# Kernel optimization log

Hardware: AMD Instinct MI355X
Metric: run time of the kernel (lower is better)

Reference implementation:

```python
import jax, jax.numpy as jnp
import numpy as np

NH, NKV, D = 8, 2, 256
EPS = 1e-6
SCALING = 1.0 / 256.0  # query_rescale_scalar / query_pre_attn_scalar


def _rms(x):
    # Gemma3nRMSNorm with with_scale=False: x / sqrt(mean(x^2) + eps)
    return x * jax.lax.rsqrt(jnp.mean(x * x, axis=-1, keepdims=True) + EPS)


def _rotate_half(x):
    h = x.shape[-1] // 2
    return jnp.concatenate([-x[..., h:], x[..., :h]], axis=-1)


def setup_inputs() -> dict:
    key = jax.random.key(0)
    ks = jax.random.split(key, 5)
    S, H = 4096, 2048
    hidden_states = jax.random.normal(ks[0], (S, H), dtype=jnp.float32)
    # realistic rope cos/sin
    pos = jnp.arange(S, dtype=jnp.float32)
    inv_freq = 1.0 / (10000.0 ** (jnp.arange(0, D, 2, dtype=jnp.float32) / D))
    ang = pos[:, None] * inv_freq[None, :]              # [S, D/2]
    emb = jnp.concatenate([ang, ang], axis=-1)          # [S, D]
    cos = jnp.cos(emb)
    sin = jnp.sin(emb)
    qkv_w = jax.random.normal(ks[1], ((NH + 2 * NKV) * D, H), dtype=jnp.float32) * 0.02
    o_w = jax.random.normal(ks[2], (H, NH * D), dtype=jnp.float32) * 0.02
    return {"hidden_states": hidden_states, "cos": cos, "sin": sin,
            "qkv_w": qkv_w, "o_w": o_w}


def reference(hidden_states, cos, sin, qkv_w, o_w):
    S = hidden_states.shape[0]
    qkv = hidden_states @ qkv_w.T                        # [S, (NH+2NKV)*D]
    q, k, v = jnp.split(qkv, [NH * D, (NH + NKV) * D], axis=-1)
    q = q.reshape(S, NH, D)                              # [S, NH, D]
    k = k.reshape(S, NKV, D)
    v = v.reshape(S, NKV, D)
    # per-head RMSNorm (no learned scale) on q, k, v
    q = _rms(q)
    k = _rms(k)
    v = _rms(v)
    # RoPE on q, k (v untouched)
    c = cos[:, None, :]
    s = sin[:, None, :]
    q = q * c + _rotate_half(q) * s
    k = k * c + _rotate_half(k) * s
    # GQA: expand kv heads to query heads
    rep = NH // NKV
    k = jnp.repeat(k, rep, axis=1)                       # [S, NH, D]
    v = jnp.repeat(v, rep, axis=1)
    scores = jnp.einsum('qhd,khd->hqk', q, k) * SCALING  # [NH, S, S]
    mask = jnp.tril(jnp.ones((S, S), dtype=bool))
    scores = jnp.where(mask[None], scores, jnp.finfo(scores.dtype).min)
    probs = jax.nn.softmax(scores, axis=-1)
    attn = jnp.einsum('hqk,khd->qhd', probs, v)          # [S, NH, D]
    out = attn.reshape(S, NH * D) @ o_w.T                # [S, H]
    return out
```

## Files before the change

kernel.cpp:

```cpp
#include <hip/hip_runtime.h>

#define NHEADS 8
#define NKVH   2
#define HD     256
#define SEQ    4096
#define HID    2048
#define QKVN   3072
#define SCAL   (1.0f/256.0f)
#define NITEMS 640

typedef __attribute__((ext_vector_type(8))) __bf16 bf16x8;
typedef __attribute__((ext_vector_type(4))) float  f32x4;

__device__ __forceinline__ unsigned short f2bf(float f) {
  unsigned int u = __builtin_bit_cast(unsigned int, f);
  u += 0x7fffu + ((u >> 16) & 1u);
  return (unsigned short)(u >> 16);
}
__device__ __forceinline__ float bf2f(unsigned short b) {
  return __builtin_bit_cast(float, (unsigned int)b << 16);
}

__device__ __forceinline__ void async_copy16(const void* g, void* l) {
  __builtin_amdgcn_global_load_lds(
      (__attribute__((address_space(1))) void*)(g),
      (__attribute__((address_space(3))) void*)(l), 16, 0, 0);
}

__device__ __forceinline__ int slot_prefix(int b) {
  if (b < 16) return 0;
  if (b < 32) return b - 16;
  if (b < 48) return 16 + 2 * (b - 32);
  return 48 + 3 * (b - 48);
}

__global__ __launch_bounds__(256) void cvt_bf16(const float* __restrict__ in,
                                                unsigned short* __restrict__ out,
                                                int n4) {
  int i = blockIdx.x * 256 + threadIdx.x;
  if (i >= n4) return;
  float4 v = reinterpret_cast<const float4*>(in)[i];
  ushort4 o;
  o.x = f2bf(v.x); o.y = f2bf(v.y); o.z = f2bf(v.z); o.w = f2bf(v.w);
  reinterpret_cast<ushort4*>(out)[i] = o;
}

template <bool OUT_BF16>
__global__ __launch_bounds__(256) void gemm_bt(const unsigned short* __restrict__ A,
                                               const unsigned short* __restrict__ B,
                                               void* __restrict__ C,
                                               int M, int N, int K) {
  __shared__ __align__(16) unsigned short Als[128 * 64];
  __shared__ __align__(16) unsigned short Bls[128 * 64];
  const int t    = threadIdx.x;
  const int lane = t & 63;
  const int wid  = t >> 6;
  const int wr = wid >> 1, wc = wid & 1;
  const int l15 = lane & 15, lg = lane >> 4;
  const int m0 = blockIdx.y * 128, n0 = blockIdx.x * 128;

  f32x4 acc[4][4] = {};

  for (int k0 = 0; k0 < K; k0 += 64) {
    __syncthreads();
#pragma unroll
    for (int i = 0; i < 4; ++i) {
      int c   = i * 256 + t;
      int kc  = c >> 9;
      int row = (c >> 2) & 127;
      int j8  = (c & 3) ^ (row & 3);
      int gcol = k0 + kc * 32 + j8 * 8;
      async_copy16(A + (size_t)(m0 + row) * K + gcol, Als + c * 8);
      async_copy16(B + (size_t)(n0 + row) * K + gcol, Bls + c * 8);
    }
    __syncthreads();
#pragma unroll
    for (int kc = 0; kc < 2; ++kc) {
      bf16x8 af[4], bfr[4];
#pragma unroll
      for (int m = 0; m < 4; ++m) {
        int row   = wr * 64 + m * 16 + l15;
        int chunk = kc * 512 + row * 4 + (lg ^ (row & 3));
        af[m] = *reinterpret_cast<const bf16x8*>(Als + chunk * 8);
      }
#pragma unroll
      for (int n = 0; n < 4; ++n) {
        int row   = wc * 64 + n * 16 + l15;
        int chunk = kc * 512 + row * 4 + (lg ^ (row & 3));
        bfr[n] = *reinterpret_cast<const bf16x8*>(Bls + chunk * 8);
      }
#pragma unroll
      for (int m = 0; m < 4; ++m)
#pragma unroll
        for (int n = 0; n < 4; ++n)
          acc[m][n] = __builtin_amdgcn_mfma_f32_16x16x32_bf16(af[m], bfr[n],
                                                              acc[m][n], 0, 0, 0);
    }
  }

#pragma unroll
  for (int m = 0; m < 4; ++m) {
#pragma unroll
    for (int n = 0; n < 4; ++n) {
      int col = n0 + wc * 64 + n * 16 + l15;
#pragma unroll
      for (int r = 0; r < 4; ++r) {
        int rowg = m0 + wr * 64 + m * 16 + lg * 4 + r;
        if constexpr (OUT_BF16)
          reinterpret_cast<unsigned short*>(C)[(size_t)rowg * N + col] =
              f2bf(acc[m][n][r]);
        else
          reinterpret_cast<float*>(C)[(size_t)rowg * N + col] = acc[m][n][r];
      }
    }
  }
}

__global__ __launch_bounds__(256) void postproc(const unsigned short* __restrict__ qkv,
                                                const float* __restrict__ cosb,
                                                const float* __restrict__ sinb,
                                                unsigned short* __restrict__ q,
                                                unsigned short* __restrict__ k,
                                                unsigned short* __restrict__ vt) {
  const int wid = threadIdx.x >> 6, lane = threadIdx.x & 63;
  const int task = blockIdx.x * 4 + wid;
  const int s = task / 12, comp = task % 12;

  ushort4 raw = reinterpret_cast<const ushort4*>(qkv + (size_t)task * 256)[lane];
  float x0 = bf2f(raw.x), x1 = bf2f(raw.y), x2 = bf2f(raw.z), x3 = bf2f(raw.w);

  float ss = x0 * x0 + x1 * x1 + x2 * x2 + x3 * x3;
#pragma unroll
  for (int m = 1; m < 64; m <<= 1) ss += __shfl_xor(ss, m);
  float inv = rsqrtf(ss * (1.0f / 256.0f) + 1e-6f);
  x0 *= inv; x1 *= inv; x2 *= inv; x3 *= inv;

  if (comp < 10) {
    float4 c  = reinterpret_cast<const float4*>(cosb + (size_t)s * 256)[lane];
    float4 sn = reinterpret_cast<const float4*>(sinb + (size_t)s * 256)[lane];
    float p0 = __shfl_xor(x0, 32), p1 = __shfl_xor(x1, 32);
    float p2 = __shfl_xor(x2, 32), p3 = __shfl_xor(x3, 32);
    float sg = (lane < 32) ? -1.0f : 1.0f;
    x0 = x0 * c.x + sg * p0 * sn.x;
    x1 = x1 * c.y + sg * p1 * sn.y;
    x2 = x2 * c.z + sg * p2 * sn.z;
    x3 = x3 * c.w + sg * p3 * sn.w;
  }

  if (comp < 8) {
    ushort4 o;
    o.x = f2bf(x0 * SCAL); o.y = f2bf(x1 * SCAL);
    o.z = f2bf(x2 * SCAL); o.w = f2bf(x3 * SCAL);
    reinterpret_cast<ushort4*>(q + ((size_t)s * NHEADS + comp) * 256)[lane] = o;
  } else if (comp < 10) {
    ushort4 o;
    o.x = f2bf(x0); o.y = f2bf(x1); o.z = f2bf(x2); o.w = f2bf(x3);
    reinterpret_cast<ushort4*>(k + ((size_t)(comp - 8) * SEQ + s) * 256)[lane] = o;
  } else {
    size_t base = (size_t)(comp - 10) * 1048576 + (size_t)(s >> 5) * 8192 +
                  (size_t)((s >> 3) & 3) * 2048 + (s & 7);
    int d0 = lane * 4;
    vt[base + (size_t)(d0 + 0) * 8] = f2bf(x0);
    vt[base + (size_t)(d0 + 1) * 8] = f2bf(x1);
    vt[base + (size_t)(d0 + 2) * 8] = f2bf(x2);
    vt[base + (size_t)(d0 + 3) * 8] = f2bf(x3);
  }
}

__global__ __launch_bounds__(256, 2) void flash(const unsigned short* __restrict__ q,
                                                const unsigned short* __restrict__ k,
                                                const unsigned short* __restrict__ vtg,
                                                unsigned short* __restrict__ attn,
                                                unsigned short* __restrict__ opart,
                                                float* __restrict__ ml0,
                                                float* __restrict__ mlp,
                                                int* __restrict__ ticket) {
  extern __shared__ __align__(16) unsigned short lds[];
  unsigned short* Kls = lds;
  unsigned short* Vls = lds + 16384;
  unsigned short* Pls = lds + 32768;
  __shared__ int s_item;

  const int tid  = threadIdx.x;
  const int lane = tid & 63, wid = tid >> 6;
  const int l15 = lane & 15, lg = lane >> 4;

  for (;;) {
    if (tid == 0) s_item = atomicAdd(ticket, 1);
    __syncthreads();
    const int it = s_item;
    __syncthreads();
    if (it >= NITEMS) break;

    int b, hp, j;
    if (it < 256)      { b = 63 - (it >> 4);          int r = it & 15;        hp = r >> 2; j = r & 3; }
    else if (it < 448) { int u = it - 256; b = 47 - u / 12; int r = u % 12;   hp = r / 3;  j = r % 3; }
    else if (it < 576) { int u = it - 448; b = 31 - (u >> 3); int r = u & 7;  hp = r >> 1; j = r & 1; }
    else               { int u = it - 576; b = 15 - (u >> 2); hp = u & 3;     j = 0; }

    const int h0 = hp * 2, kvh = hp >> 1;
    const int total_t = 2 * b + 2;
    const int t0 = j * 32;
    const int t1 = min(t0 + 32, total_t) - 1;
    const int qb = b * 64 + wid * 16;

    const unsigned short* kbase  = k   + (size_t)kvh * SEQ * 256;
    const unsigned short* vstage = vtg + (size_t)kvh * 1048576;

    bf16x8 qf[2][8];
#pragma unroll
    for (int g = 0; g < 2; ++g) {
      const unsigned short* qrow =
          q + ((size_t)(qb + l15) * NHEADS + h0 + g) * 256 + lg * 8;
#pragma unroll
      for (int kc = 0; kc < 8; ++kc)
        qf[g][kc] = *reinterpret_cast<const bf16x8*>(qrow + kc * 32);
    }

    f32x4 o[16][2];
#pragma unroll
    for (int i = 0; i < 16; ++i)
#pragma unroll
      for (int g = 0; g < 2; ++g) o[i][g] = f32x4{0.f, 0.f, 0.f, 0.f};
    float mr0 = -1e30f, lr0 = 0.f, mr1 = -1e30f, lr1 = 0.f;

    auto stage = [&](int bb, int t) {
      const int kvb = t * 32;
#pragma unroll
      for (int i = 0; i < 4; ++i) {
        int p = i * 256 + tid;
        int krow = p >> 5, pj = p & 31;
        int jj = (pj & ~7) | ((pj ^ krow) & 7);
        async_copy16(kbase + (size_t)(kvb + krow) * 256 + jj * 8,
                     Kls + bb * 8192 + p * 8);
      }
      const unsigned short* vsrc = vstage + (size_t)t * 8192;
#pragma unroll
      for (int i = 0; i < 4; ++i) {
        int p = i * 256 + tid;
        async_copy16(vsrc + p * 8, Vls + bb * 8192 + p * 8);
      }
    };

    int cur = 0;
    stage(0, t0);
    __syncthreads();

    for (int t = t0; t <= t1; ++t) {
      const int kvb = t * 32;
      if (t + 1 <= t1) stage(cur ^ 1, t + 1);

      if (kvb <= qb + 15) {
        const unsigned short* Kc = Kls + cur * 8192;
        const unsigned short* Vc = Vls + cur * 8192;

        f32x4 s[2][2] = {};
        __builtin_amdgcn_s_setprio(1);
#pragma unroll
        for (int n = 0; n < 2; ++n) {
          const int row = n * 16 + l15;
#pragma unroll
          for (int kc = 0; kc < 8; ++kc) {
            int jj = kc * 4 + lg;
            int pj = (jj & ~7) | ((jj ^ row) & 7);
            bf16x8 kf = *reinterpret_cast<const bf16x8*>(Kc + (row * 32 + pj) * 8);
            s[0][n] = __builtin_amdgcn_mfma_f32_16x16x32_bf16(kf, qf[0][kc], s[0][n], 0, 0, 0);
            s[1][n] = __builtin_amdgcn_mfma_f32_16x16x32_bf16(kf, qf[1][kc], s[1][n], 0, 0, 0);
          }
        }
        __builtin_amdgcn_s_setprio(0);

        if (kvb + 31 > qb) {
#pragma unroll
          for (int n = 0; n < 2; ++n)
#pragma unroll
            for (int r = 0; r < 4; ++r)
              if (kvb + n * 16 + lg * 4 + r > qb + l15) {
                s[0][n][r] = -1e30f;
                s[1][n][r] = -1e30f;
              }
        }

        float pm0 = fmaxf(fmaxf(fmaxf(s[0][0][0], s[0][0][1]), fmaxf(s[0][0][2], s[0][0][3])),
                          fmaxf(fmaxf(s[0][1][0], s[0][1][1]), fmaxf(s[0][1][2], s[0][1][3])));
        float pm1 = fmaxf(fmaxf(fmaxf(s[1][0][0], s[1][0][1]), fmaxf(s[1][0][2], s[1][0][3])),
                          fmaxf(fmaxf(s[1][1][0], s[1][1][1]), fmaxf(s[1][1][2], s[1][1][3])));
        pm0 = fmaxf(pm0, __shfl_xor(pm0, 16));
        pm0 = fmaxf(pm0, __shfl_xor(pm0, 32));
        pm1 = fmaxf(pm1, __shfl_xor(pm1, 16));
        pm1 = fmaxf(pm1, __shfl_xor(pm1, 32));

        if (__any(fmaxf(pm0 - mr0, pm1 - mr1) > 8.0f)) {
          float mn0 = fmaxf(mr0, pm0), mn1 = fmaxf(mr1, pm1);
          float sc0 = __expf(mr0 - mn0), sc1 = __expf(mr1 - mn1);
#pragma unroll
          for (int i = 0; i < 16; ++i)
#pragma unroll
            for (int r = 0; r < 4; ++r) {
              o[i][0][r] *= sc0;
              o[i][1][r] *= sc1;
            }
          lr0 *= sc0; lr1 *= sc1;
          mr0 = mn0;  mr1 = mn1;
        }

#pragma unroll
        for (int n = 0; n < 2; ++n)
#pragma unroll
          for (int r = 0; r < 4; ++r) {
            s[0][n][r] = __expf(s[0][n][r] - mr0);
            s[1][n][r] = __expf(s[1][n][r] - mr1);
          }

        float rs0 = ((s[0][0][0] + s[0][0][1]) + (s[0][0][2] + s[0][0][3])) +
                    ((s[0][1][0] + s[0][1][1]) + (s[0][1][2] + s[0][1][3]));
        float rs1 = ((s[1][0][0] + s[1][0][1]) + (s[1][0][2] + s[1][0][3])) +
                    ((s[1][1][0] + s[1][1][1]) + (s[1][1][2] + s[1][1][3]));
        rs0 += __shfl_xor(rs0, 16); rs0 += __shfl_xor(rs0, 32);
        rs1 += __shfl_xor(rs1, 16); rs1 += __shfl_xor(rs1, 32);
        lr0 += rs0; lr1 += rs1;

#pragma unroll
        for (int g = 0; g < 2; ++g) {
          unsigned short* Pr = Pls + ((wid * 2 + g) * 16 + l15) * 40;
#pragma unroll
          for (int n = 0; n < 2; ++n) {
            ushort4 w;
            w.x = f2bf(s[g][n][0]); w.y = f2bf(s[g][n][1]);
            w.z = f2bf(s[g][n][2]); w.w = f2bf(s[g][n][3]);
            *reinterpret_cast<ushort4*>(Pr + n * 16 + lg * 4) = w;
          }
        }
        asm volatile("s_waitcnt lgkmcnt(0)" ::: "memory");
        __builtin_amdgcn_sched_barrier(0);

        bf16x8 pb0 = *reinterpret_cast<const bf16x8*>(
            Pls + ((wid * 2 + 0) * 16 + l15) * 40 + lg * 8);
        bf16x8 pb1 = *reinterpret_cast<const bf16x8*>(
            Pls + ((wid * 2 + 1) * 16 + l15) * 40 + lg * 8);
        __builtin_amdgcn_s_setprio(1);
#pragma unroll
        for (int dt = 0; dt < 16; ++dt) {
          bf16x8 vf = *reinterpret_cast<const bf16x8*>(
              Vc + ((lg << 8) + dt * 16 + l15) * 8);
          o[dt][0] = __builtin_amdgcn_mfma_f32_16x16x32_bf16(vf, pb0, o[dt][0], 0, 0, 0);
          o[dt][1] = __builtin_amdgcn_mfma_f32_16x16x32_bf16(vf, pb1, o[dt][1], 0, 0, 0);
        }
        __builtin_amdgcn_s_setprio(0);
      }

      __syncthreads();
      cur ^= 1;
    }

    const int qrow = qb + l15;
#pragma unroll
    for (int g = 0; g < 2; ++g) {
      const int head = h0 + g;
      const float mg = g ? mr1 : mr0;
      const float lg_ = g ? lr1 : lr0;
      if (j == 0) {
#pragma unroll
        for (int dt = 0; dt < 16; ++dt) {
          ushort4 w;
          w.x = f2bf(o[dt][g][0]); w.y = f2bf(o[dt][g][1]);
          w.z = f2bf(o[dt][g][2]); w.w = f2bf(o[dt][g][3]);
          *reinterpret_cast<ushort4*>(
              attn + (size_t)qrow * HID + head * 256 + dt * 16 + lg * 4) = w;
        }
        if (lg == 0)
          reinterpret_cast<float2*>(ml0)[head * SEQ + qrow] = float2{mg, lg_};
      } else {
        const int p = slot_prefix(b) + (j - 1);
        const size_t prow = ((size_t)head * 96 + p) * 64 + (qrow & 63);
#pragma unroll
        for (int dt = 0; dt < 16; ++dt) {
          ushort4 w;
          w.x = f2bf(o[dt][g][0]); w.y = f2bf(o[dt][g][1]);
          w.z = f2bf(o[dt][g][2]); w.w = f2bf(o[dt][g][3]);
          *reinterpret_cast<ushort4*>(opart + prow * 256 + dt * 16 + lg * 4) = w;
        }
        if (lg == 0) reinterpret_cast<float2*>(mlp)[prow] = float2{mg, lg_};
      }
    }
    __syncthreads();
  }
}

__global__ __launch_bounds__(256) void merge(const unsigned short* __restrict__ opart,
                                             const float* __restrict__ ml0,
                                             const float* __restrict__ mlp,
                                             unsigned short* __restrict__ attn) {
  const int wid = threadIdx.x >> 6, lane = threadIdx.x & 63;
  const int rid = blockIdx.x * 4 + wid;
  const int h = rid >> 12, s = rid & 4095;
  const int b = s >> 6;
  const int n = (b >> 4) + 1;

  float2 m_l[4];
  m_l[0] = reinterpret_cast<const float2*>(ml0)[rid];
  const int pf = slot_prefix(b);
  size_t prow[4];
  for (int jj = 1; jj < n; ++jj) {
    prow[jj] = ((size_t)h * 96 + pf + jj - 1) * 64 + (s & 63);
    m_l[jj] = reinterpret_cast<const float2*>(mlp)[prow[jj]];
  }

  float M = m_l[0].x;
  for (int jj = 1; jj < n; ++jj) M = fmaxf(M, m_l[jj].x);
  float w[4], L = 0.f;
  for (int jj = 0; jj < n; ++jj) {
    w[jj] = __expf(m_l[jj].x - M);
    L += w[jj] * m_l[jj].y;
  }
  float invL = 1.0f / L;
  for (int jj = 0; jj < n; ++jj) w[jj] *= invL;

  unsigned short* arow = attn + (size_t)s * HID + h * 256;
  ushort4 a = reinterpret_cast<const ushort4*>(arow)[lane];
  float acc0 = w[0] * bf2f(a.x), acc1 = w[0] * bf2f(a.y);
  float acc2 = w[0] * bf2f(a.z), acc3 = w[0] * bf2f(a.w);
  for (int jj = 1; jj < n; ++jj) {
    ushort4 bq = reinterpret_cast<const ushort4*>(opart + prow[jj] * 256)[lane];
    acc0 += w[jj] * bf2f(bq.x); acc1 += w[jj] * bf2f(bq.y);
    acc2 += w[jj] * bf2f(bq.z); acc3 += w[jj] * bf2f(bq.w);
  }
  ushort4 o;
  o.x = f2bf(acc0); o.y = f2bf(acc1); o.z = f2bf(acc2); o.w = f2bf(acc3);
  reinterpret_cast<ushort4*>(arow)[lane] = o;
}

extern "C" void kernel_launch(void* const* d_in, const int* in_sizes, int n_in,
                              void* d_out, int out_size, void* d_ws, size_t ws_size,
                              hipStream_t stream) {
  const float* hs   = (const float*)d_in[0];
  const float* cosb = (const float*)d_in[1];
  const float* sinb = (const float*)d_in[2];
  const float* qkvw = (const float*)d_in[3];
  const float* ow   = (const float*)d_in[4];

  char* ws = (char*)d_ws;
  unsigned short* hs_bf   = (unsigned short*)(ws + 0);
  unsigned short* wqkv_bf = (unsigned short*)(ws + 16777216);
  unsigned short* wo_bf   = (unsigned short*)(ws + 29360128);
  unsigned short* qkv_bf  = (unsigned short*)(ws + 37748736);
  unsigned short* attn_bf = qkv_bf;
  unsigned short* q_bf    = (unsigned short*)(ws + 62914560);
  unsigned short* k_bf    = (unsigned short*)(ws + 79691776);
  unsigned short* vt_bf   = (unsigned short*)(ws + 83886080);
  unsigned short* opart   = (unsigned short*)(ws + 0);
  float*          ml0buf  = (float*)(ws + 25165824);
  float*          mlpbuf  = (float*)(ws + 25427968);
  int*            ticket  = (int*)(ws + 25821184);

  cvt_bf16<<<dim3((SEQ * HID / 4 + 255) / 256), dim3(256), 0, stream>>>(hs, hs_bf, SEQ * HID / 4);
  cvt_bf16<<<dim3((QKVN * HID / 4 + 255) / 256), dim3(256), 0, stream>>>(qkvw, wqkv_bf, QKVN * HID / 4);
  cvt_bf16<<<dim3((HID * HID / 4 + 255) / 256), dim3(256), 0, stream>>>(ow, wo_bf, HID * HID / 4);

  gemm_bt<true><<<dim3(QKVN / 128, SEQ / 128), dim3(256), 0, stream>>>(
      hs_bf, wqkv_bf, qkv_bf, SEQ, QKVN, HID);

  postproc<<<dim3(SEQ * 12 / 4), dim3(256), 0, stream>>>(qkv_bf, cosb, sinb, q_bf, k_bf, vt_bf);

  hipMemsetAsync(ticket, 0, 4, stream);

  flash<<<dim3(512), dim3(256), 75776, stream>>>(q_bf, k_bf, vt_bf, attn_bf,
                                                 opart, ml0buf, mlpbuf, ticket);

  merge<<<dim3(8192), dim3(256), 0, stream>>>(opart, ml0buf, mlpbuf, attn_bf);

  gemm_bt<false><<<dim3(HID / 128, SEQ / 128), dim3(256), 0, stream>>>(
      attn_bf, wo_bf, d_out, SEQ, HID, HID);
}
```

Measured before the change: 345.4 us.

## Split work queue per KV head and defer softmax row reductions

```diff
diff --git a/kernel.cpp b/kernel.cpp
--- a/kernel.cpp
+++ b/kernel.cpp
@@ -7,7 +7,7 @@
 #define HID    2048
 #define QKVN   3072
 #define SCAL   (1.0f/256.0f)
-#define NITEMS 640
+#define NITEMS_SIDE 320
 
 typedef __attribute__((ext_vector_type(8))) __bf16 bf16x8;
 typedef __attribute__((ext_vector_type(4))) float  f32x4;
@@ -184,28 +184,30 @@
   const int tid  = threadIdx.x;
   const int lane = tid & 63, wid = tid >> 6;
   const int l15 = lane & 15, lg = lane >> 4;
+  const int side = (blockIdx.x & 7) >> 2;
+  const int kvh = side;
+
+  const unsigned short* kbase  = k   + (size_t)kvh * SEQ * 256;
+  const unsigned short* vstage = vtg + (size_t)kvh * 1048576;
 
   for (;;) {
-    if (tid == 0) s_item = atomicAdd(ticket, 1);
+    __syncthreads();
+    if (tid == 0) s_item = atomicAdd(ticket + side, 1);
     __syncthreads();
     const int it = s_item;
-    __syncthreads();
-    if (it >= NITEMS) break;
-
-    int b, hp, j;
-    if (it < 256)      { b = 63 - (it >> 4);          int r = it & 15;        hp = r >> 2; j = r & 3; }
-    else if (it < 448) { int u = it - 256; b = 47 - u / 12; int r = u % 12;   hp = r / 3;  j = r % 3; }
-    else if (it < 576) { int u = it - 448; b = 31 - (u >> 3); int r = u & 7;  hp = r >> 1; j = r & 1; }
-    else               { int u = it - 576; b = 15 - (u >> 2); hp = u & 3;     j = 0; }
-
-    const int h0 = hp * 2, kvh = hp >> 1;
+    if (it >= NITEMS_SIDE) break;
+
+    int b, hpl, j;
+    if (it < 128)      { b = 63 - (it >> 3);             int r = it & 7; hpl = r >> 2; j = r & 3; }
+    else if (it < 224) { int u = it - 128; b = 47 - u / 6; int r = u % 6; hpl = r / 3;  j = r % 3; }
+    else if (it < 288) { int u = it - 224; b = 31 - (u >> 2); int r = u & 3; hpl = r >> 1; j = r & 1; }
+    else               { int u = it - 288; b = 15 - (u >> 1); hpl = u & 1; j = 0; }
+
+    const int h0 = kvh * 4 + hpl * 2;
     const int total_t = 2 * b + 2;
     const int t0 = j * 32;
     const int t1 = min(t0 + 32, total_t) - 1;
     const int qb = b * 64 + wid * 16;
-
-    const unsigned short* kbase  = k   + (size_t)kvh * SEQ * 256;
-    const unsigned short* vstage = vtg + (size_t)kvh * 1048576;
 
     bf16x8 qf[2][8];
 #pragma unroll
@@ -285,14 +287,14 @@
                           fmaxf(fmaxf(s[0][1][0], s[0][1][1]), fmaxf(s[0][1][2], s[0][1][3])));
         float pm1 = fmaxf(fmaxf(fmaxf(s[1][0][0], s[1][0][1]), fmaxf(s[1][0][2], s[1][0][3])),
                           fmaxf(fmaxf(s[1][1][0], s[1][1][1]), fmaxf(s[1][1][2], s[1][1][3])));
-        pm0 = fmaxf(pm0, __shfl_xor(pm0, 16));
-        pm0 = fmaxf(pm0, __shfl_xor(pm0, 32));
-        pm1 = fmaxf(pm1, __shfl_xor(pm1, 16));
-        pm1 = fmaxf(pm1, __shfl_xor(pm1, 32));
 
         if (__any(fmaxf(pm0 - mr0, pm1 - mr1) > 8.0f)) {
-          float mn0 = fmaxf(mr0, pm0), mn1 = fmaxf(mr1, pm1);
-          float sc0 = __expf(mr0 - mn0), sc1 = __expf(mr1 - mn1);
+          float q0 = fmaxf(mr0, pm0), q1 = fmaxf(mr1, pm1);
+          q0 = fmaxf(q0, __shfl_xor(q0, 16));
+          q0 = fmaxf(q0, __shfl_xor(q0, 32));
+          q1 = fmaxf(q1, __shfl_xor(q1, 16));
+          q1 = fmaxf(q1, __shfl_xor(q1, 32));
+          float sc0 = __expf(mr0 - q0), sc1 = __expf(mr1 - q1);
 #pragma unroll
           for (int i = 0; i < 16; ++i)
 #pragma unroll
@@ -301,7 +303,7 @@
               o[i][1][r] *= sc1;
             }
           lr0 *= sc0; lr1 *= sc1;
-          mr0 = mn0;  mr1 = mn1;
+          mr0 = q0;   mr1 = q1;
         }
 
 #pragma unroll
@@ -312,13 +314,10 @@
             s[1][n][r] = __expf(s[1][n][r] - mr1);
           }
 
-        float rs0 = ((s[0][0][0] + s[0][0][1]) + (s[0][0][2] + s[0][0][3])) +
-                    ((s[0][1][0] + s[0][1][1]) + (s[0][1][2] + s[0][1][3]));
-        float rs1 = ((s[1][0][0] + s[1][0][1]) + (s[1][0][2] + s[1][0][3])) +
-                    ((s[1][1][0] + s[1][1][1]) + (s[1][1][2] + s[1][1][3]));
-        rs0 += __shfl_xor(rs0, 16); rs0 += __shfl_xor(rs0, 32);
-        rs1 += __shfl_xor(rs1, 16); rs1 += __shfl_xor(rs1, 32);
-        lr0 += rs0; lr1 += rs1;
+        lr0 += ((s[0][0][0] + s[0][0][1]) + (s[0][0][2] + s[0][0][3])) +
+               ((s[0][1][0] + s[0][1][1]) + (s[0][1][2] + s[0][1][3]));
+        lr1 += ((s[1][0][0] + s[1][0][1]) + (s[1][0][2] + s[1][0][3])) +
+               ((s[1][1][0] + s[1][1][1]) + (s[1][1][2] + s[1][1][3]));
 
 #pragma unroll
         for (int g = 0; g < 2; ++g) {
@@ -353,6 +352,9 @@
       cur ^= 1;
     }
 
+    lr0 += __shfl_xor(lr0, 16); lr0 += __shfl_xor(lr0, 32);
+    lr1 += __shfl_xor(lr1, 16); lr1 += __shfl_xor(lr1, 32);
+
     const int qrow = qb + l15;
 #pragma unroll
     for (int g = 0; g < 2; ++g) {
@@ -383,7 +385,6 @@
         if (lg == 0) reinterpret_cast<float2*>(mlp)[prow] = float2{mg, lg_};
       }
     }
-    __syncthreads();
   }
 }
 
@@ -462,7 +463,7 @@
 
   postproc<<<dim3(SEQ * 12 / 4), dim3(256), 0, stream>>>(qkv_bf, cosb, sinb, q_bf, k_bf, vt_bf);
 
-  hipMemsetAsync(ticket, 0, 4, stream);
+  hipMemsetAsync(ticket, 0, 8, stream);
 
   flash<<<dim3(512), dim3(256), 75776, stream>>>(q_bf, k_bf, vt_bf, attn_bf,
                                                  opart, ml0buf, mlpbuf, ticket);
```

Result: faster. 327.6 us (-5.2%).
